# Kernel tuning notes

Hardware: AMD Instinct MI355X
Metric: run time of the kernel (lower is better)

Reference implementation:

```python
import jax, jax.numpy as jnp
import numpy as np

TAU = 0.1
NUM_HEADS = 8
HEAD_DIMS = 64


def setup_inputs() -> dict:
    key = jax.random.key(0)
    ks = jax.random.split(key, 5)
    B, T, D = 4, 1024, 512
    H, Dh = NUM_HEADS, HEAD_DIMS
    x = jax.random.normal(ks[0], (B, T, D), dtype=jnp.float32)
    scale = 1.0 / np.sqrt(D)
    wq = jax.random.normal(ks[1], (D, H * Dh), dtype=jnp.float32) * scale
    wk = jax.random.normal(ks[2], (D, H * Dh), dtype=jnp.float32) * scale
    wv = jax.random.normal(ks[3], (D, H * Dh), dtype=jnp.float32) * scale
    wo = jax.random.normal(ks[4], (H * Dh, D // H), dtype=jnp.float32) * scale
    return {"x": x, "wq": wq, "wk": wk, "wv": wv, "wo": wo}


def _scan_score(a, tau):
    # a: [B,H,T,T] soft-match scores; tau > 0 branch of _rosa_qkv_scan_score
    T = a.shape[-1]
    r = jnp.arange(T)
    future = r[:, None] < r[None, :]                       # [T,T], True above diag
    a = jnp.where(future[None, None], 0.0, a)
    # rotate columns: out[...,i,j] = a[...,i,(i+j+1) % T]
    c1 = (r[:, None] + r[None, :] + 1) % T                 # [T,T]
    a = jnp.take_along_axis(a, c1[None, None], axis=-1)
    cs = jnp.cumsum(a, axis=-2)                            # cumsum over rows i
    a = cs - jax.lax.cummax(cs * (1.0 - a), axis=2)        # run-length style scan
    # rotate back: out[...,i,j] = a[...,i,(j-i+T-1) % T]
    c2 = (r[None, :] - r[:, None] + T - 1) % T
    a = jnp.take_along_axis(a, c2[None, None], axis=-1)
    return a


def _attn_score(a, tau):
    # tau > 0 branch of _rosa_qkv_attn_score: positional tie-break + causal softmax
    T = a.shape[-1]
    r = jnp.arange(T)
    p = r.astype(a.dtype)
    pos = p[None, :] / (p[:, None] + 1.0)                  # p[i,j] = j/(i+1)
    future = r[:, None] < r[None, :]
    a = jnp.where(future[None, None], -jnp.inf, a + pos[None, None])
    return jax.nn.softmax(a / tau, axis=-1)


def reference(x, wq, wk, wv, wo):
    B, T, D = x.shape
    H, Dh = NUM_HEADS, HEAD_DIMS
    tau = TAU
    iq = (x @ wq).reshape(B, T, H, Dh)
    ik = (x @ wk).reshape(B, T, H, Dh)
    iv = (x @ wv).reshape(B, T, H, Dh)
    iq_sm = jax.nn.softmax(iq / tau, axis=-1).astype(jnp.float32)
    ik_sm = jax.nn.softmax(ik / tau, axis=-1).astype(jnp.float32)
    iv_sm = jax.nn.softmax(iv / tau, axis=-1).astype(jnp.float32)
    # match scores [B,H,T,T]
    a = jnp.einsum("bihd,bjhd->bhij", iq_sm, ik_sm)
    a = _scan_score(a, tau)
    a = _attn_score(a, tau)
    o = jnp.einsum("bhij,bjhd->bhid", a, iv_sm)            # [B,H,T,Dh]
    xv = wo.reshape(H, Dh, D // H)
    o = jnp.einsum("bhid,hde->bhie", o, xv)                # [B,H,T,D//H]
    return o.transpose(0, 2, 1, 3).reshape(B, T, D)
```

## Files before the change

kernel.cpp:

```cpp
#include <hip/hip_runtime.h>
#include <math.h>

#define BB    4
#define TT    1024
#define DD    512
#define NH    8
#define DH    64
#define BH    32
#define INV_TAU 10.0f

typedef __attribute__((ext_vector_type(8))) short short8;
typedef __attribute__((ext_vector_type(4))) float f4;
typedef __attribute__((ext_vector_type(8))) _Float16 half8;

__device__ inline unsigned short f2bf(float f) {
  unsigned u = __float_as_uint(f);
  u += 0x7FFFu + ((u >> 16) & 1u);
  return (unsigned short)(u >> 16);
}
__device__ inline float bf2f(unsigned short h) {
  return __uint_as_float(((unsigned)h) << 16);
}

__global__ __launch_bounds__(256) void k_prep(
    const float* __restrict__ x, const float* __restrict__ wq,
    const float* __restrict__ wk, const float* __restrict__ wv,
    unsigned short* __restrict__ xh, unsigned short* __restrict__ xl,
    unsigned short* __restrict__ wth, unsigned short* __restrict__ wtl)
{
  __shared__ float Wf[64][65];
  const int blk = blockIdx.x;
  const int tid = threadIdx.x;
  if (blk < 2048) {
    const int i = (blk * 256 + tid) * 4;
    float4 v = *(const float4*)&x[i];
    ushort4 h, l;
    h.x = f2bf(v.x); l.x = f2bf(v.x - bf2f(h.x));
    h.y = f2bf(v.y); l.y = f2bf(v.y - bf2f(h.y));
    h.z = f2bf(v.z); l.z = f2bf(v.z - bf2f(h.z));
    h.w = f2bf(v.w); l.w = f2bf(v.w - bf2f(h.w));
    *(ushort4*)&xh[i] = h;
    *(ushort4*)&xl[i] = l;
    return;
  }
  const int b = blk - 2048;
  const int ten = b >> 6;
  const int r = b & 63;
  const int n0 = (r & 7) * 64, k0 = (r >> 3) * 64;
  const float* W = (ten == 0) ? wq : ((ten == 1) ? wk : wv);
#pragma unroll
  for (int p = 0; p < 4; ++p) {
    int kk = p * 16 + (tid >> 4);
    int nn = (tid & 15) * 4;
    float4 v = *(const float4*)&W[(size_t)(k0 + kk) * 512 + n0 + nn];
    Wf[kk][nn + 0] = v.x; Wf[kk][nn + 1] = v.y;
    Wf[kk][nn + 2] = v.z; Wf[kk][nn + 3] = v.w;
  }
  __syncthreads();
  const int n = tid >> 2, kq = tid & 3;
  size_t base = ((size_t)(ten * 512 + n0 + n)) * 512 + k0 + kq * 16;
#pragma unroll
  for (int jj = 0; jj < 4; ++jj) {
    ushort4 h, l;
    float f0 = Wf[kq * 16 + jj * 4 + 0][n];
    float f1 = Wf[kq * 16 + jj * 4 + 1][n];
    float f2 = Wf[kq * 16 + jj * 4 + 2][n];
    float f3 = Wf[kq * 16 + jj * 4 + 3][n];
    h.x = f2bf(f0); l.x = f2bf(f0 - bf2f(h.x));
    h.y = f2bf(f1); l.y = f2bf(f1 - bf2f(h.y));
    h.z = f2bf(f2); l.z = f2bf(f2 - bf2f(h.z));
    h.w = f2bf(f3); l.w = f2bf(f3 - bf2f(h.w));
    *(ushort4*)&wth[base + jj * 4] = h;
    *(ushort4*)&wtl[base + jj * 4] = l;
  }
}

__global__ __launch_bounds__(256) void k_proj_mfma(
    const unsigned short* __restrict__ xh, const unsigned short* __restrict__ xl,
    const unsigned short* __restrict__ wth, const unsigned short* __restrict__ wtl,
    unsigned short* __restrict__ qh, unsigned short* __restrict__ ql,
    unsigned short* __restrict__ kh, unsigned short* __restrict__ kl,
    float* __restrict__ vs)
{
  __shared__ unsigned short Ah[64][40];
  __shared__ unsigned short Al[64][40];
  __shared__ unsigned short Bh[128][40];
  __shared__ unsigned short Bl[128][40];
  const int tid = threadIdx.x;
  const int n0g = blockIdx.x * 128;
  const int m0 = blockIdx.y * 64;
  const int w = tid >> 6, lane = tid & 63;
  const int mw = (w & 1) * 32, nw = (w >> 1) * 64;
  const int quad = lane >> 4, l16 = lane & 15;
  const int srow = tid >> 2;
  const int sk = (tid & 3) * 8;

  f4 acc[2][4] = {};

  for (int k0 = 0; k0 < DD; k0 += 32) {
    short8 a0 = *(const short8*)&xh[(size_t)(m0 + srow) * DD + k0 + sk];
    short8 a1 = *(const short8*)&xl[(size_t)(m0 + srow) * DD + k0 + sk];
    short8 b0 = *(const short8*)&wth[(size_t)(n0g + srow) * DD + k0 + sk];
    short8 b1 = *(const short8*)&wth[(size_t)(n0g + 64 + srow) * DD + k0 + sk];
    short8 b2 = *(const short8*)&wtl[(size_t)(n0g + srow) * DD + k0 + sk];
    short8 b3 = *(const short8*)&wtl[(size_t)(n0g + 64 + srow) * DD + k0 + sk];
    *(short8*)&Ah[srow][sk] = a0;
    *(short8*)&Al[srow][sk] = a1;
    *(short8*)&Bh[srow][sk] = b0;  *(short8*)&Bh[64 + srow][sk] = b1;
    *(short8*)&Bl[srow][sk] = b2;  *(short8*)&Bl[64 + srow][sk] = b3;
    __syncthreads();

    short8 fbh[4], fbl[4];
#pragma unroll
    for (int nt = 0; nt < 4; ++nt) {
      fbh[nt] = *(const short8*)&Bh[nw + nt * 16 + l16][quad * 8];
      fbl[nt] = *(const short8*)&Bl[nw + nt * 16 + l16][quad * 8];
    }
#pragma unroll
    for (int mt = 0; mt < 2; ++mt) {
      short8 fah = *(const short8*)&Ah[mw + mt * 16 + l16][quad * 8];
      short8 fal = *(const short8*)&Al[mw + mt * 16 + l16][quad * 8];
#pragma unroll
      for (int nt = 0; nt < 4; ++nt) {
        acc[mt][nt] = __builtin_amdgcn_mfma_f32_16x16x32_bf16(fah, fbh[nt], acc[mt][nt], 0, 0, 0);
        acc[mt][nt] = __builtin_amdgcn_mfma_f32_16x16x32_bf16(fah, fbl[nt], acc[mt][nt], 0, 0, 0);
        acc[mt][nt] = __builtin_amdgcn_mfma_f32_16x16x32_bf16(fal, fbh[nt], acc[mt][nt], 0, 0, 0);
      }
    }
    __syncthreads();
  }

  const int tensor = n0g >> 9;
  const int ncol = (n0g & 511) + nw;
  const int h = ncol >> 6;
#pragma unroll
  for (int mt = 0; mt < 2; ++mt) {
#pragma unroll
    for (int r = 0; r < 4; ++r) {
      float v0 = acc[mt][0][r], v1 = acc[mt][1][r];
      float v2 = acc[mt][2][r], v3 = acc[mt][3][r];
      float mx = fmaxf(fmaxf(v0, v1), fmaxf(v2, v3));
#pragma unroll
      for (int msk = 1; msk <= 8; msk <<= 1) mx = fmaxf(mx, __shfl_xor(mx, msk, 64));
      float e0 = __expf((v0 - mx) * INV_TAU);
      float e1 = __expf((v1 - mx) * INV_TAU);
      float e2 = __expf((v2 - mx) * INV_TAU);
      float e3 = __expf((v3 - mx) * INV_TAU);
      float sm = e0 + e1 + e2 + e3;
#pragma unroll
      for (int msk = 1; msk <= 8; msk <<= 1) sm += __shfl_xor(sm, msk, 64);
      float inv = 1.0f / sm;
      int row = m0 + mw + mt * 16 + quad * 4 + r;
      int b = row >> 10, t = row & 1023;
      size_t base = (((size_t)b * NH + h) * TT + t) * DH;
      float e[4] = {e0 * inv, e1 * inv, e2 * inv, e3 * inv};
      if (tensor == 2) {
#pragma unroll
        for (int c = 0; c < 4; ++c) vs[base + l16 + c * 16] = e[c];
      } else {
        unsigned short* oh = tensor ? kh : qh;
        unsigned short* ol = tensor ? kl : ql;
#pragma unroll
        for (int c = 0; c < 4; ++c) {
          unsigned short hh = f2bf(e[c]);
          oh[base + l16 + c * 16] = hh;
          ol[base + l16 + c * 16] = f2bf(e[c] - bf2f(hh));
        }
      }
    }
  }
}

__global__ __launch_bounds__(256) void k_qkv(
    const unsigned short* __restrict__ qh, const unsigned short* __restrict__ ql,
    const unsigned short* __restrict__ kh, const unsigned short* __restrict__ kl,
    _Float16* __restrict__ A, const float* __restrict__ vs,
    unsigned short* __restrict__ vth, unsigned short* __restrict__ vtl)
{
  __shared__ float Vf[64][65];
  const int tid = threadIdx.x;
  if (blockIdx.x >= 1088) {
    const int b = blockIdx.x - 1088;
    const int z = b & 31, t0 = (b >> 5) * 64;
#pragma unroll
    for (int it = 0; it < 4; ++it) {
      int tl = it * 16 + (tid >> 4);
      int d4 = (tid & 15) * 4;
      float4 v = *(const float4*)&vs[((size_t)z * TT + t0 + tl) * DH + d4];
      Vf[tl][d4 + 0] = v.x; Vf[tl][d4 + 1] = v.y;
      Vf[tl][d4 + 2] = v.z; Vf[tl][d4 + 3] = v.w;
    }
    __syncthreads();
#pragma unroll
    for (int it = 0; it < 8; ++it) {
      int d = it * 8 + (tid >> 5);
      int t = (tid & 31) * 2;
      float a0 = Vf[t][d], a1 = Vf[t + 1][d];
      unsigned short h0 = f2bf(a0), h1 = f2bf(a1);
      unsigned short l0 = f2bf(a0 - bf2f(h0)), l1 = f2bf(a1 - bf2f(h1));
      size_t o = ((size_t)z * DH + d) * TT + t0 + t;
      ushort2 hh; hh.x = h0; hh.y = h1;
      ushort2 ll; ll.x = l0; ll.y = l1;
      *(ushort2*)&vth[o] = hh;
      *(ushort2*)&vtl[o] = ll;
    }
    return;
  }
  const int gid = blockIdx.x * 4 + (tid >> 6);
  const int z = gid / 136;
  const int lx = gid - z * 136;
  int ti = (int)((sqrtf(8.0f * lx + 1.0f) - 1.0f) * 0.5f);
  while ((ti + 1) * (ti + 2) / 2 <= lx) ++ti;
  while (ti * (ti + 1) / 2 > lx) --ti;
  const int tj = lx - ti * (ti + 1) / 2;
  const int i0 = ti * 64, j0 = tj * 64;
  const int lane = tid & 63;
  const int quad = lane >> 4, l16 = lane & 15;
  const size_t zb = (size_t)z * TT * DH;

  short8 fbh[4][2], fbl[4][2];
#pragma unroll
  for (int nt = 0; nt < 4; ++nt)
#pragma unroll
    for (int ks = 0; ks < 2; ++ks) {
      size_t o = zb + (size_t)(j0 + nt * 16 + l16) * DH + ks * 32 + quad * 8;
      fbh[nt][ks] = *(const short8*)&kh[o];
      fbl[nt][ks] = *(const short8*)&kl[o];
    }

  f4 acc[4][4] = {};
#pragma unroll
  for (int mt = 0; mt < 4; ++mt) {
    short8 fah[2], fal[2];
#pragma unroll
    for (int ks = 0; ks < 2; ++ks) {
      size_t o = zb + (size_t)(i0 + mt * 16 + l16) * DH + ks * 32 + quad * 8;
      fah[ks] = *(const short8*)&qh[o];
      fal[ks] = *(const short8*)&ql[o];
    }
#pragma unroll
    for (int nt = 0; nt < 4; ++nt)
#pragma unroll
      for (int ks = 0; ks < 2; ++ks) {
        acc[mt][nt] = __builtin_amdgcn_mfma_f32_16x16x32_bf16(fah[ks], fbh[nt][ks], acc[mt][nt], 0, 0, 0);
        acc[mt][nt] = __builtin_amdgcn_mfma_f32_16x16x32_bf16(fah[ks], fbl[nt][ks], acc[mt][nt], 0, 0, 0);
        acc[mt][nt] = __builtin_amdgcn_mfma_f32_16x16x32_bf16(fal[ks], fbh[nt][ks], acc[mt][nt], 0, 0, 0);
      }
  }

  _Float16* Ab = A + (size_t)z * TT * TT;
#pragma unroll
  for (int mt = 0; mt < 4; ++mt)
#pragma unroll
    for (int nt = 0; nt < 4; ++nt)
#pragma unroll
      for (int r = 0; r < 4; ++r)
        Ab[(size_t)(i0 + mt * 16 + quad * 4 + r) * TT + j0 + nt * 16 + l16] =
            (_Float16)acc[mt][nt][r];
}

__global__ __launch_bounds__(1024) void k_scan(_Float16* __restrict__ A)
{
  __shared__ float Ssum[16][64];
  __shared__ float Gmax[16][64];
  const int blk = blockIdx.x;
  const int p = blk >> 5;
  const int xb = (p < 8) ? p : (23 - p);
  const int z = blk & 31;
  const int lane = threadIdx.x & 63;
  const int w = threadIdx.x >> 6;
  _Float16* __restrict__ Ab = A + (size_t)z * TT * TT;
  const int dbase = xb * 64;
  const int d = dbase + lane;
  const int L = (TT - dbase) >> 4;
  const int r0 = dbase + w * L;

  float S = 0.0f;
#pragma unroll 8
  for (int t = 0; t < L; ++t) {
    int i = r0 + t;
    size_t idx = (i >= d) ? ((size_t)i * (TT + 1) - d) : 0;
    float s = (float)Ab[idx];
    S += (i >= d) ? s : 0.0f;
  }
  Ssum[w][lane] = S;
  __syncthreads();

  float cs_in = 0.0f;
  for (int ww = 0; ww < w; ++ww) cs_in += Ssum[ww][lane];

  {
    float lcs = 0.0f, gm = 0.0f;
#pragma unroll 8
    for (int t = 0; t < L; ++t) {
      int i = r0 + t;
      size_t idx = (i >= d) ? ((size_t)i * (TT + 1) - d) : 0;
      float s0 = (float)Ab[idx];
      float s = (i >= d) ? s0 : 0.0f;
      lcs += s;
      gm = fmaxf(gm, (cs_in + lcs) * (1.0f - s));
    }
    Gmax[w][lane] = gm;
  }
  __syncthreads();

  float m = 0.0f;
  for (int ww = 0; ww < w; ++ww) m = fmaxf(m, Gmax[ww][lane]);

  {
    float lcs = 0.0f;
#pragma unroll 8
    for (int t = 0; t < L; ++t) {
      int i = r0 + t;
      bool ok = (i >= d);
      size_t idx = ok ? ((size_t)i * (TT + 1) - d) : 0;
      float s0 = (float)Ab[idx];
      float s = ok ? s0 : 0.0f;
      lcs += s;
      float cs = cs_in + lcs;
      m = fmaxf(m, cs * (1.0f - s));
      if (ok) Ab[idx] = (_Float16)(cs - m);
    }
  }
}

__global__ __launch_bounds__(64) void k_pv(
    const _Float16* __restrict__ A, const unsigned short* __restrict__ vth,
    const unsigned short* __restrict__ vtl, float* __restrict__ oatt,
    float* __restrict__ Opart, float* __restrict__ ml)
{
  const int lane = threadIdx.x;
  const int quad = lane >> 4, l16 = lane & 15;
  const int blk = blockIdx.x;
  const int z = blk & 31;
  const int item = blk >> 5;
  int ti, band, jt0, jt1, chunk;
  bool split;
  if (item < 32) {
    ti = 8 + (item >> 2); band = item & 3; jt0 = 0; jt1 = 8; chunk = 0; split = true;
  } else {
    int i2 = item - 32;
    int l = 8 - (i2 >> 3);
    int sub = i2 & 7;
    band = sub & 3;
    if (sub < 4) { ti = l + 7; jt0 = 8; jt1 = ti + 1; chunk = 1; split = true; }
    else         { ti = l - 1; jt0 = 0; jt1 = ti + 1; chunk = 0; split = false; }
  }
  const _Float16* Az = A + (size_t)z * TT * TT;
  const unsigned short* vh = vth + (size_t)z * DH * TT;
  const unsigned short* vl = vtl + (size_t)z * DH * TT;

  const int i0 = ti * 64;
  const int irow = i0 + band * 16 + l16;
  const float invi = 1.0f / (float)(irow + 1);
  f4 acc[4] = {};
  float m_old = -3e38f, l_run = 0.0f;

  float posu[16];
#pragma unroll
  for (int u = 0; u < 16; ++u)
    posu[u] = (float)((u >> 3) * 32 + quad * 8 + (u & 7)) * invi;
  const float jstep = 64.0f * invi;
  float jtoff = (float)jt0 * jstep;

  for (int jt = jt0; jt < jt1; ++jt) {
    const bool masked = (jt == ti);
    float sc[16];
#pragma unroll
    for (int ks = 0; ks < 2; ++ks) {
      half8 hv = *(const half8*)&Az[(size_t)irow * TT + jt * 64 + ks * 32 + quad * 8];
#pragma unroll
      for (int u = 0; u < 8; ++u) sc[ks * 8 + u] = (float)hv[u];
    }
#pragma unroll
    for (int u = 0; u < 16; ++u) {
      float v = sc[u] + (jtoff + posu[u]);
      int j = jt * 64 + (u >> 3) * 32 + quad * 8 + (u & 7);
      sc[u] = (masked && j > irow) ? -3e38f : v;
    }
    float mt_ = sc[0];
#pragma unroll
    for (int u = 1; u < 16; ++u) mt_ = fmaxf(mt_, sc[u]);
    mt_ = fmaxf(mt_, __shfl_xor(mt_, 16, 64));
    mt_ = fmaxf(mt_, __shfl_xor(mt_, 32, 64));
    float m_new = fmaxf(m_old, mt_);
    float alpha = __expf((m_old - m_new) * INV_TAU);
    unsigned short ph[16], pl[16];
    float ls = 0.0f;
#pragma unroll
    for (int u = 0; u < 16; ++u) {
      float pvv = __expf((sc[u] - m_new) * INV_TAU);
      unsigned short hh = f2bf(pvv);
      ph[u] = hh; pl[u] = f2bf(pvv - bf2f(hh));
      ls += pvv;
    }
    ls += __shfl_xor(ls, 16, 64);
    ls += __shfl_xor(ls, 32, 64);
    l_run = l_run * alpha + ls;
    m_old = m_new;
#pragma unroll
    for (int rr = 0; rr < 4; ++rr) {
      float ar = __shfl(alpha, quad * 4 + rr, 64);
#pragma unroll
      for (int nt = 0; nt < 4; ++nt) acc[nt][rr] *= ar;
    }
#pragma unroll
    for (int ks = 0; ks < 2; ++ks) {
      short8 pah, pal;
#pragma unroll
      for (int u = 0; u < 8; ++u) { pah[u] = (short)ph[ks * 8 + u]; pal[u] = (short)pl[ks * 8 + u]; }
#pragma unroll
      for (int nt = 0; nt < 4; ++nt) {
        size_t vo = (size_t)(nt * 16 + l16) * TT + jt * 64 + ks * 32 + quad * 8;
        short8 fvh = *(const short8*)&vh[vo];
        short8 fvl = *(const short8*)&vl[vo];
        acc[nt] = __builtin_amdgcn_mfma_f32_16x16x32_bf16(pah, fvh, acc[nt], 0, 0, 0);
        acc[nt] = __builtin_amdgcn_mfma_f32_16x16x32_bf16(pah, fvl, acc[nt], 0, 0, 0);
        acc[nt] = __builtin_amdgcn_mfma_f32_16x16x32_bf16(pal, fvh, acc[nt], 0, 0, 0);
      }
    }
    jtoff += jstep;
  }

  if (!split) {
#pragma unroll
    for (int rr = 0; rr < 4; ++rr) {
      float lr = __shfl(l_run, quad * 4 + rr, 64);
      float inv = 1.0f / lr;
      int orow = i0 + band * 16 + quad * 4 + rr;
#pragma unroll
      for (int nt = 0; nt < 4; ++nt)
        oatt[((size_t)z * TT + orow) * DH + nt * 16 + l16] = acc[nt][rr] * inv;
    }
  } else {
    if (quad == 0) {
      int prow = i0 + band * 16 + l16 - 512;
      size_t mo = (((size_t)chunk * 32 + z) * 512 + prow) * 2;
      ml[mo + 0] = m_old;
      ml[mo + 1] = l_run;
    }
#pragma unroll
    for (int rr = 0; rr < 4; ++rr) {
      int prow = i0 + band * 16 + quad * 4 + rr - 512;
      size_t po = (((size_t)chunk * 32 + z) * 512 + prow) * 64;
#pragma unroll
      for (int nt = 0; nt < 4; ++nt)
        Opart[po + nt * 16 + l16] = acc[nt][rr];
    }
  }
}

__global__ __launch_bounds__(256) void k_oproj(
    const float* __restrict__ oatt, const float* __restrict__ wo,
    const float* __restrict__ Opart, const float* __restrict__ ml,
    float* __restrict__ out)
{
  __shared__ float Wl[64][64];
  __shared__ float Ol[16][64];
  const int z = blockIdx.y;
  const int t0 = blockIdx.x * 16;
  const int b = z >> 3, h = z & 7;
  const int tid = threadIdx.x;
  const float* wb = wo + (size_t)h * 64 * 64;
#pragma unroll
  for (int u = 0; u < 4; ++u) {
    int q = tid + 256 * u;
    int dd = q >> 4, e4 = (q & 15) * 4;
    *(float4*)&Wl[dd][e4] = *(const float4*)&wb[(size_t)dd * 64 + e4];
  }
  {
    int rr = tid >> 4, d4 = (tid & 15) * 4;
    int trow = t0 + rr;
    if (trow < 512) {
      *(float4*)&Ol[rr][d4] = *(const float4*)&oatt[((size_t)z * TT + trow) * DH + d4];
    } else {
      int pr = trow - 512;
      size_t m0o = (((size_t)0 * 32 + z) * 512 + pr) * 2;
      size_t m1o = (((size_t)1 * 32 + z) * 512 + pr) * 2;
      float m0 = ml[m0o], l0 = ml[m0o + 1];
      float m1 = ml[m1o], l1 = ml[m1o + 1];
      float mm = fmaxf(m0, m1);
      float w0 = __expf((m0 - mm) * INV_TAU);
      float w1 = __expf((m1 - mm) * INV_TAU);
      float inv = 1.0f / (l0 * w0 + l1 * w1);
      float4 o0 = *(const float4*)&Opart[(((size_t)0 * 32 + z) * 512 + pr) * 64 + d4];
      float4 o1 = *(const float4*)&Opart[(((size_t)1 * 32 + z) * 512 + pr) * 64 + d4];
      Ol[rr][d4 + 0] = (o0.x * w0 + o1.x * w1) * inv;
      Ol[rr][d4 + 1] = (o0.y * w0 + o1.y * w1) * inv;
      Ol[rr][d4 + 2] = (o0.z * w0 + o1.z * w1) * inv;
      Ol[rr][d4 + 3] = (o0.w * w0 + o1.w * w1) * inv;
    }
  }
  __syncthreads();
  const int rg = tid >> 6, e = tid & 63;
  float a0 = 0, a1 = 0, a2 = 0, a3 = 0;
#pragma unroll
  for (int dd = 0; dd < 64; ++dd) {
    float wv = Wl[dd][e];
    a0 += Ol[rg * 4 + 0][dd] * wv;
    a1 += Ol[rg * 4 + 1][dd] * wv;
    a2 += Ol[rg * 4 + 2][dd] * wv;
    a3 += Ol[rg * 4 + 3][dd] * wv;
  }
  size_t ob = ((size_t)b * TT + t0 + rg * 4) * DD + h * 64 + e;
  out[ob] = a0; out[ob + DD] = a1; out[ob + 2 * DD] = a2; out[ob + 3 * DD] = a3;
}

extern "C" void kernel_launch(void* const* d_in, const int* in_sizes, int n_in,
                              void* d_out, int out_size, void* d_ws, size_t ws_size,
                              hipStream_t stream)
{
  (void)in_sizes; (void)n_in; (void)out_size; (void)ws_size;
  const float* x  = (const float*)d_in[0];
  const float* wq = (const float*)d_in[1];
  const float* wk = (const float*)d_in[2];
  const float* wv = (const float*)d_in[3];
  const float* wo = (const float*)d_in[4];
  float* out = (float*)d_out;

  char* ws = (char*)d_ws;
  const size_t MB = 1024 * 1024;
  unsigned short* qh = (unsigned short*)(ws);
  unsigned short* ql = (unsigned short*)(ws + 4 * MB);
  unsigned short* kh = (unsigned short*)(ws + 8 * MB);
  unsigned short* kl = (unsigned short*)(ws + 12 * MB);
  float*          vs = (float*)(ws + 16 * MB);
  unsigned short* vth = (unsigned short*)(ws + 24 * MB);
  unsigned short* vtl = (unsigned short*)(ws + 28 * MB);
  float*          oatt = (float*)(ws);
  _Float16*       A  = (_Float16*)(ws + 33 * MB);
  unsigned short* xh = (unsigned short*)(ws + 33 * MB);
  unsigned short* xl = (unsigned short*)(ws + 37 * MB);
  float*          Opart = (float*)(ws + 97 * MB);
  float*          ml = (float*)(ws + 113 * MB);
  unsigned short* wth = (unsigned short*)(ws + 161 * MB);
  unsigned short* wtl = (unsigned short*)(ws + 161 * MB + 1536 * 1024);

  hipLaunchKernelGGL(k_prep, dim3(2048 + 192), dim3(256), 0, stream,
                     x, wq, wk, wv, xh, xl, wth, wtl);
  hipLaunchKernelGGL(k_proj_mfma, dim3(12, 64), dim3(256), 0, stream,
                     xh, xl, wth, wtl, qh, ql, kh, kl, vs);
  hipLaunchKernelGGL(k_qkv, dim3(1088 + 512), dim3(256), 0, stream,
                     qh, ql, kh, kl, A, vs, vth, vtl);
  hipLaunchKernelGGL(k_scan, dim3(512), dim3(1024), 0, stream, A);
  hipLaunchKernelGGL(k_pv, dim3(3072), dim3(64), 0, stream, A, vth, vtl,
                     oatt, Opart, ml);
  hipLaunchKernelGGL(k_oproj, dim3(64, 32), dim3(256), 0, stream,
                     oatt, wo, Opart, ml, out);
}
```

Before: 214.5 us.

## Cache scan diagonal values in registers across the three passes

The scan kernel used to read each diagonal element from global memory three times, once per pass (sum, group max, final write). It now loads each thread's segment once into a 32-entry register array and reuses it for all three passes. Long diagonals are split into two sequential segments that carry the running sum and running max between them, so the register array stays bounded. This cuts global reads by about two thirds, in exchange for higher register pressure, an extra pair of barriers for the two-segment case, and 32-bit index arithmetic.

```diff
diff --git a/kernel.cpp b/kernel.cpp
--- a/kernel.cpp
+++ b/kernel.cpp
@@ -272,55 +272,75 @@
   _Float16* __restrict__ Ab = A + (size_t)z * TT * TT;
   const int dbase = xb * 64;
   const int d = dbase + lane;
-  const int L = (TT - dbase) >> 4;
-  const int r0 = dbase + w * L;
-
-  float S = 0.0f;
-#pragma unroll 8
-  for (int t = 0; t < L; ++t) {
-    int i = r0 + t;
-    size_t idx = (i >= d) ? ((size_t)i * (TT + 1) - d) : 0;
-    float s = (float)Ab[idx];
-    S += (i >= d) ? s : 0.0f;
-  }
-  Ssum[w][lane] = S;
-  __syncthreads();
-
-  float cs_in = 0.0f;
-  for (int ww = 0; ww < w; ++ww) cs_in += Ssum[ww][lane];
-
-  {
-    float lcs = 0.0f, gm = 0.0f;
-#pragma unroll 8
-    for (int t = 0; t < L; ++t) {
-      int i = r0 + t;
-      size_t idx = (i >= d) ? ((size_t)i * (TT + 1) - d) : 0;
-      float s0 = (float)Ab[idx];
-      float s = (i >= d) ? s0 : 0.0f;
-      lcs += s;
-      gm = fmaxf(gm, (cs_in + lcs) * (1.0f - s));
-    }
-    Gmax[w][lane] = gm;
-  }
-  __syncthreads();
-
-  float m = 0.0f;
-  for (int ww = 0; ww < w; ++ww) m = fmaxf(m, Gmax[ww][lane]);
-
-  {
-    float lcs = 0.0f;
-#pragma unroll 8
-    for (int t = 0; t < L; ++t) {
-      int i = r0 + t;
-      bool ok = (i >= d);
-      size_t idx = ok ? ((size_t)i * (TT + 1) - d) : 0;
-      float s0 = (float)Ab[idx];
-      float s = ok ? s0 : 0.0f;
-      lcs += s;
-      float cs = cs_in + lcs;
-      m = fmaxf(m, cs * (1.0f - s));
-      if (ok) Ab[idx] = (_Float16)(cs - m);
-    }
+  const int R = TT - dbase;
+  const int nseg = (R > 512) ? 2 : 1;
+  const int Ls = R / (nseg * 16);
+
+  float cs_carry = 0.0f, m_carry = 0.0f;
+  for (int sg = 0; sg < nseg; ++sg) {
+    const int r0 = dbase + sg * (R / nseg) + w * Ls;
+    const int off0 = r0 * (TT + 1) - d;
+
+    float v[32];
+    float S = 0.0f;
+#pragma unroll
+    for (int t = 0; t < 32; ++t) {
+      if (t < Ls) {
+        float s0 = (float)Ab[off0 + t * (TT + 1)];
+        float s = ((r0 + t) >= d) ? s0 : 0.0f;
+        v[t] = s;
+        S += s;
+      }
+    }
+    Ssum[w][lane] = S;
+    __syncthreads();
+
+    float cs_in = cs_carry;
+    float tot = cs_carry;
+    for (int ww = 0; ww < 16; ++ww) {
+      float sv = Ssum[ww][lane];
+      cs_in += (ww < w) ? sv : 0.0f;
+      tot += sv;
+    }
+
+    {
+      float lcs = 0.0f, gm = 0.0f;
+#pragma unroll
+      for (int t = 0; t < 32; ++t) {
+        if (t < Ls) {
+          float s = v[t];
+          lcs += s;
+          float cs = cs_in + lcs;
+          gm = fmaxf(gm, cs * (1.0f - s));
+        }
+      }
+      Gmax[w][lane] = gm;
+    }
+    __syncthreads();
+
+    float m = m_carry;
+    float mtot = m_carry;
+    for (int ww = 0; ww < 16; ++ww) {
+      float gv = Gmax[ww][lane];
+      m = fmaxf(m, (ww < w) ? gv : 0.0f);
+      mtot = fmaxf(mtot, gv);
+    }
+
+    {
+      float lcs = 0.0f;
+#pragma unroll
+      for (int t = 0; t < 32; ++t) {
+        if (t < Ls) {
+          float s = v[t];
+          lcs += s;
+          float cs = cs_in + lcs;
+          m = fmaxf(m, cs * (1.0f - s));
+          if ((r0 + t) >= d) Ab[off0 + t * (TT + 1)] = (_Float16)(cs - m);
+        }
+      }
+    }
+    cs_carry = tot;
+    m_carry = mtot;
   }
 }
 
```

Result: slower. 224.9 us (+4.9%).
